# Kernel optimization log

Hardware: AMD Instinct MI355X
Metric: run time of the kernel (lower is better)

## Reference

```python
import jax, jax.numpy as jnp
import numpy as np

DIM = 64
HEADS = 8
GLOBAL_HEADS = 4   # heads - local_attn_heads
DIM_HEAD = 64
INNER = HEADS * DIM_HEAD  # 512
NB_FEATURES = int(DIM_HEAD * np.log(DIM_HEAD))  # 266, performer_pytorch default
NUM_TOKENS = 64
VOCAB = 26
B, N = 8, 2048


def _orth_gauss(m, d, rng):
    # gaussian orthogonal random matrix (scaling=0), as in performer_pytorch
    blocks = []
    for _ in range(int(np.ceil(m / d))):
        q, _ = np.linalg.qr(rng.normal(size=(d, d)))
        blocks.append(q.T)
    mat = np.concatenate(blocks, 0)[:m]
    mult = np.linalg.norm(rng.normal(size=(m, d)), axis=1)
    return (mult[:, None] * mat).astype(np.float32)


def _layernorm(x, g, b, eps=1e-5):
    mu = x.mean(-1, keepdims=True)
    var = jnp.mean((x - mu) ** 2, axis=-1, keepdims=True)
    return (x - mu) / jnp.sqrt(var + eps) * g + b


def _fixed_pos_emb(n, dim):
    inv_freq = 1.0 / (10000.0 ** (jnp.arange(0, dim, 2, dtype=jnp.float32) / dim))
    t = jnp.arange(n, dtype=jnp.float32)[:, None] * inv_freq[None, :]
    return jnp.concatenate([jnp.sin(t), jnp.cos(t)], axis=-1)  # [n, dim]


def _rotate_every_two(x):
    x1, x2 = x[..., ::2], x[..., 1::2]
    return jnp.stack((-x2, x1), axis=-1).reshape(x.shape)


def _apply_rotary(q, k, sinu):
    half = sinu.shape[-1] // 2
    sin = jnp.repeat(sinu[:, :half], 2, axis=-1)
    cos = jnp.repeat(sinu[:, half:], 2, axis=-1)
    rot = lambda t: t * cos + _rotate_every_two(t) * sin
    return rot(q), rot(k)


def _softmax_kernel(x, proj, is_query, eps=1e-4):
    # FAVOR+ positive softmax random features
    dn = x.shape[-1] ** -0.25
    ratio = proj.shape[0] ** -0.5
    dash = jnp.einsum('bhnd,md->bhnm', x * dn, proj)
    diag = jnp.sum(x * x, axis=-1, keepdims=True) * (0.5 * dn * dn)
    mx = jnp.max(dash, axis=-1, keepdims=True) if is_query else jnp.max(dash)
    return ratio * (jnp.exp(dash - diag - mx) + eps)


def _forward(input_ids, tok_emb, ln1_g, ln1_b, Wq, Wk, Wv, Wo, ln2_g, ln2_b,
             W1, b1, W2, b2, lnf_g, lnf_b, Wout, bout, Wc1, bc1, Wc2, bc2, proj):
    b, n = input_ids.shape
    mask = input_ids != 0  # padding mask (pad id == 0)
    x = tok_emb[input_ids] + _fixed_pos_emb(n, DIM)[None]  # token + abs sinusoidal pos
    sinu = _fixed_pos_emb(n, DIM_HEAD)  # rotary table for attention heads

    def attn(h):
        hn = _layernorm(h, ln1_g, ln1_b)
        to_h = lambda W: (hn @ W).reshape(b, n, HEADS, DIM_HEAD).transpose(0, 2, 1, 3)
        q, k, v = to_h(Wq), to_h(Wk), to_h(Wv)  # [b,h,n,d]
        qg, ql = q[:, :GLOBAL_HEADS], q[:, GLOBAL_HEADS:]
        kg, kl = k[:, :GLOBAL_HEADS], k[:, GLOBAL_HEADS:]
        vg, vl = v[:, :GLOBAL_HEADS], v[:, GLOBAL_HEADS:]
        # --- global heads: FAVOR+ linear attention (rotary applied to global q/k only) ---
        vg = vg * mask[:, None, :, None]  # performer zeroes v at padded positions
        qg, kg = _apply_rotary(qg, kg, sinu)
        qp = _softmax_kernel(qg, proj, True)   # [b,h,n,m]
        kp = _softmax_kernel(kg, proj, False)
        ctx = jnp.einsum('bhnm,bhnd->bhmd', kp, vg)
        denom = jnp.einsum('bhnm,bhm->bhn', qp, kp.sum(axis=2))
        og = jnp.einsum('bhnm,bhmd->bhnd', qp, ctx) / denom[..., None]
        # --- local heads: window_size == seq_len -> exact softmax attn + key pad mask ---
        dots = jnp.einsum('bhnd,bhmd->bhnm', ql, kl) * (DIM_HEAD ** -0.5)
        dots = jnp.where(mask[:, None, None, :], dots, jnp.asarray(-1e9, dots.dtype))
        ol = jnp.einsum('bhnm,bhmd->bhnd', jax.nn.softmax(dots, axis=-1), vl)
        out = jnp.concatenate([og, ol], axis=1).transpose(0, 2, 1, 3).reshape(b, n, INNER)
        return out @ Wo

    def ff(h):
        hn = _layernorm(h, ln2_g, ln2_b)
        return jax.nn.gelu(hn @ W1 + b1, approximate=False) @ W2 + b2

    # reversible sequence, depth 1: x1 = x2 = x; output = mean of the two streams
    y1 = x + attn(x)
    y2 = x + ff(y1)
    h = _layernorm(0.5 * (y1 + y2), lnf_g, lnf_b)
    logits = h @ Wout + bout  # [b, n, NUM_TOKENS]
    rep = logits[:, 0, :]     # CLS slot, [b, 64]
    out = jax.nn.relu(rep @ Wc1 + bc1) @ Wc2 + bc2  # [b, 2]
    return out, rep


def setup_inputs():
    key = jax.random.key(0)
    ks = jax.random.split(key, 12)
    rng = np.random.default_rng(0)
    s = lambda k, shape, scale=0.05: jax.random.normal(k, shape, jnp.float32) * scale
    return {
        'input_ids': jax.random.randint(ks[0], (B, N), 0, VOCAB, dtype=jnp.int32),
        'tok_emb': s(ks[1], (NUM_TOKENS, DIM), 1.0),
        'ln1_g': jnp.ones((DIM,), jnp.float32), 'ln1_b': jnp.zeros((DIM,), jnp.float32),
        'Wq': s(ks[2], (DIM, INNER)), 'Wk': s(ks[3], (DIM, INNER)), 'Wv': s(ks[4], (DIM, INNER)),
        'Wo': s(ks[5], (INNER, DIM)),
        'ln2_g': jnp.ones((DIM,), jnp.float32), 'ln2_b': jnp.zeros((DIM,), jnp.float32),
        'W1': s(ks[6], (DIM, 4 * DIM)), 'b1': jnp.zeros((4 * DIM,), jnp.float32),
        'W2': s(ks[7], (4 * DIM, DIM)), 'b2': jnp.zeros((DIM,), jnp.float32),
        'lnf_g': jnp.ones((DIM,), jnp.float32), 'lnf_b': jnp.zeros((DIM,), jnp.float32),
        'Wout': s(ks[8], (DIM, NUM_TOKENS)), 'bout': jnp.zeros((NUM_TOKENS,), jnp.float32),
        'Wc1': s(ks[9], (DIM, 32)), 'bc1': jnp.zeros((32,), jnp.float32),
        'Wc2': s(ks[10], (32, 2)), 'bc2': jnp.zeros((2,), jnp.float32),
        'proj': jnp.asarray(_orth_gauss(NB_FEATURES, DIM_HEAD, rng)),
    }


def reference(input_ids, tok_emb, ln1_g, ln1_b, Wq, Wk, Wv, Wo, ln2_g, ln2_b,
              W1, b1, W2, b2, lnf_g, lnf_b, Wout, bout, Wc1, bc1, Wc2, bc2, proj):
    return _forward(input_ids, tok_emb, ln1_g, ln1_b, Wq, Wk, Wv, Wo, ln2_g, ln2_b,
                    W1, b1, W2, b2, lnf_g, lnf_b, Wout, bout, Wc1, bc1, Wc2, bc2, proj)
```

## Files before the change

### kernel.cpp

```cpp
#include <hip/hip_runtime.h>
#include <math.h>

#define NTOK 2048
#define NBF 266
#define MPAD 272
#define ZWORDS4 138323u

typedef unsigned short u16;
typedef __attribute__((ext_vector_type(8))) short short8;
typedef __attribute__((ext_vector_type(4))) float f32x4;

__device__ __forceinline__ float bf2f(u16 u) {
  unsigned int x = ((unsigned int)u) << 16;
  return __uint_as_float(x);
}
__device__ __forceinline__ u16 f2bf(float f) {
  unsigned int x = __float_as_uint(f);
  unsigned int r = x + 0x7FFFu + ((x >> 16) & 1u);
  return (u16)(r >> 16);
}
__device__ __forceinline__ float wredsum64(float v) {
  for (int o = 32; o > 0; o >>= 1) v += __shfl_xor(v, o);
  return v;
}
__device__ __forceinline__ float bsum256(float v, float* red) {
  for (int o = 32; o > 0; o >>= 1) v += __shfl_xor(v, o);
  __syncthreads();
  if ((threadIdx.x & 63) == 0) red[threadIdx.x >> 6] = v;
  __syncthreads();
  return red[0] + red[1] + red[2] + red[3];
}
__device__ __forceinline__ float bmax256(float v, float* red) {
  for (int o = 32; o > 0; o >>= 1) v = fmaxf(v, __shfl_xor(v, o));
  __syncthreads();
  if ((threadIdx.x & 63) == 0) red[threadIdx.x >> 6] = v;
  __syncthreads();
  return fmaxf(fmaxf(red[0], red[1]), fmaxf(red[2], red[3]));
}
#define INVF_C 0.4152410118609190f

__global__ __launch_bounds__(128) void k_prep(
    const int* __restrict__ ids, const float* __restrict__ tok_emb,
    const float* __restrict__ ln1g, const float* __restrict__ ln1b,
    const float* __restrict__ Wk, const float* __restrict__ Wv,
    u16* __restrict__ Kg, u16* __restrict__ Vg, u16* __restrict__ hng,
    float* __restrict__ diagK, float* __restrict__ x0,
    uint4* __restrict__ zbase) {
  int blk = blockIdx.x;
  int b = blk >> 8, nt = blk & 255;
  int n0 = nt * 8;
  int t = threadIdx.x;
  int w = t >> 6, lane = t & 63;
  __shared__ float hn[8][64];
  __shared__ float idm[8];
  __shared__ float2 sctab[256];

  {
    unsigned int zi = (unsigned int)blk * 128u + (unsigned int)t;
    if (zi < ZWORDS4) zbase[zi] = make_uint4(0u, 0u, 0u, 0u);
  }
#pragma unroll
  for (int p = 0; p < 2; ++p) {
    int ee = t + p * 128;
    int n = n0 + (ee >> 5), i = ee & 31;
    float ang = (float)n * exp2f(-INVF_C * (float)i);
    sctab[ee] = make_float2(sinf(ang), cosf(ang));
  }
  __syncthreads();

  float g = ln1g[lane], bb = ln1b[lane];
#pragma unroll
  for (int j2 = 0; j2 < 4; ++j2) {
    int j = w * 4 + j2;
    int n = n0 + j;
    int id = ids[b * NTOK + n];
    float2 p = sctab[(j << 5) + (lane & 31)];
    float pv = (lane < 32) ? p.x : p.y;
    float xv = tok_emb[id * 64 + lane] + pv;
    float mu = wredsum64(xv) * 0.015625f;
    float dv = xv - mu;
    float var = wredsum64(dv * dv) * 0.015625f;
    float hv = dv * rsqrtf(var + 1e-5f) * g + bb;
    hn[j][lane] = hv;
    hng[((size_t)b * NTOK + n) * 64 + lane] = f2bf(hv);
    if (lane == 0) idm[j] = (id != 0) ? 1.f : 0.f;
    if (n == 0) x0[b * 64 + lane] = xv;
  }
  __syncthreads();

  float acc[8][4];
#pragma unroll
  for (int j = 0; j < 8; ++j)
#pragma unroll
    for (int i = 0; i < 4; ++i) acc[j][i] = 0.f;
  const float* wsrc = (t < 64) ? (Wk + t * 4) : (Wv + (t - 64) * 4);
  for (int d2 = 0; d2 < 64; ++d2) {
    float4 w0 = *reinterpret_cast<const float4*>(wsrc + d2 * 512);
#pragma unroll
    for (int j = 0; j < 8; ++j) {
      float hv = hn[j][d2];
      acc[j][0] += hv * w0.x; acc[j][1] += hv * w0.y;
      acc[j][2] += hv * w0.z; acc[j][3] += hv * w0.w;
    }
  }

  if (t < 64) {
    int hh = t >> 4, db = (t & 15) * 4;
    int i0 = (t & 15) * 2;
#pragma unroll
    for (int j = 0; j < 8; ++j) {
      int n = n0 + j;
      float2 t0 = sctab[(j << 5) + i0];
      float2 t1 = sctab[(j << 5) + i0 + 1];
      float s0 = t0.x, c0 = t0.y, s1 = t1.x, c1 = t1.y;
      float kr0 = acc[j][0] * c0 - acc[j][1] * s0;
      float kr1 = acc[j][1] * c0 + acc[j][0] * s0;
      float kr2 = acc[j][2] * c1 - acc[j][3] * s1;
      float kr3 = acc[j][3] * c1 + acc[j][2] * s1;
      float dq = kr0 * kr0 + kr1 * kr1 + kr2 * kr2 + kr3 * kr3;
      dq += __shfl_xor(dq, 1);
      dq += __shfl_xor(dq, 2);
      dq += __shfl_xor(dq, 4);
      dq += __shfl_xor(dq, 8);
      size_t hb = (size_t)(b * 4 + hh) * NTOK + n;
      if ((t & 15) == 0) diagK[hb] = dq * 0.0625f;
      ushort4 s;
      s.x = f2bf(kr0); s.y = f2bf(kr1); s.z = f2bf(kr2); s.w = f2bf(kr3);
      *reinterpret_cast<ushort4*>(Kg + hb * 64 + db) = s;
    }
  } else {
    int tv = t - 64;
    int hh = tv >> 4, db = (tv & 15) * 4;
#pragma unroll
    for (int j = 0; j < 8; ++j) {
      int n = n0 + j;
      float m = idm[j];
      ushort4 vv;
      vv.x = f2bf(acc[j][0] * m); vv.y = f2bf(acc[j][1] * m);
      vv.z = f2bf(acc[j][2] * m); vv.w = f2bf(acc[j][3] * m);
      *reinterpret_cast<ushort4*>(
          Vg + ((size_t)(b * 4 + hh) * NTOK + n) * 64 + db) = vv;
    }
  }
}

__device__ __forceinline__ void stage_prj(const float* __restrict__ proj,
                                          u16* prjbf, int t, int m0, int rows) {
  for (int c = t; c < rows * 8; c += 256) {
    int r = c >> 3, k0 = (c & 7) * 8;
    int m = m0 + r;
    int e = (r * 64 + k0) ^ ((r & 7) << 3);
    uint4 pk;
    if (m < NBF) {
      const float4* ps = reinterpret_cast<const float4*>(proj + m * 64 + k0);
      float4 p0 = ps[0], p1 = ps[1];
      pk.x = (unsigned)f2bf(p0.x) | ((unsigned)f2bf(p0.y) << 16);
      pk.y = (unsigned)f2bf(p0.z) | ((unsigned)f2bf(p0.w) << 16);
      pk.z = (unsigned)f2bf(p1.x) | ((unsigned)f2bf(p1.y) << 16);
      pk.w = (unsigned)f2bf(p1.z) | ((unsigned)f2bf(p1.w) << 16);
    } else {
      pk.x = pk.y = pk.z = pk.w = 0u;
    }
    *reinterpret_cast<uint4*>(&prjbf[e]) = pk;
  }
}

__global__ __launch_bounds__(256) void k_max(
    const u16* __restrict__ Kg, const float* __restrict__ proj,
    unsigned int* __restrict__ gmax) {
  int bh = blockIdx.x, ns = blockIdx.y;
  int t = threadIdx.x, lane = t & 63, w = t >> 6;
  __shared__ __align__(16) u16 prjbf[MPAD * 64];
  __shared__ __align__(16) u16 kbf[64 * 64];
  __shared__ float red[4];
  stage_prj(proj, prjbf, t, 0, MPAD);
  float mv = -3e38f;
  int ko = (lane >> 4) * 8;
  for (int c4 = 0; c4 < 2; ++c4) {
    int nb = ns * 128 + c4 * 64;
    __syncthreads();
    for (int p = 0; p < 2; ++p) {
      int idx = t + p * 256;
      int n = idx >> 3, k0 = (idx & 7) * 8;
      uint4 src = *reinterpret_cast<const uint4*>(
          Kg + ((size_t)bh * NTOK + nb + n) * 64 + k0);
      *reinterpret_cast<uint4*>(&kbf[(n * 64 + k0) ^ ((n & 7) << 3)]) = src;
    }
    __syncthreads();
    int nl = w * 16 + (lane & 15);
    short8 a0 = *reinterpret_cast<const short8*>(&kbf[(nl * 64 + ko) ^ ((nl & 7) << 3)]);
    short8 a1 = *reinterpret_cast<const short8*>(&kbf[(nl * 64 + ko + 32) ^ ((nl & 7) << 3)]);
#pragma unroll
    for (int mt = 0; mt < 17; ++mt) {
      int m = mt * 16 + (lane & 15);
      short8 b0 = *reinterpret_cast<const short8*>(&prjbf[(m * 64 + ko) ^ ((m & 7) << 3)]);
      short8 b1 = *reinterpret_cast<const short8*>(&prjbf[(m * 64 + ko + 32) ^ ((m & 7) << 3)]);
      f32x4 d = {0.f, 0.f, 0.f, 0.f};
      d = __builtin_amdgcn_mfma_f32_16x16x32_bf16(a0, b0, d, 0, 0, 0);
      d = __builtin_amdgcn_mfma_f32_16x16x32_bf16(a1, b1, d, 0, 0, 0);
      if (m < NBF) {
        mv = fmaxf(mv, fmaxf(fmaxf(d[0], d[1]), fmaxf(d[2], d[3])));
      }
    }
  }
  mv *= 0.35355339059327373f;
  for (int o = 32; o > 0; o >>= 1) mv = fmaxf(mv, __shfl_xor(mv, o));
  __syncthreads();
  if (lane == 0) red[w] = mv;
  __syncthreads();
  if (t == 0) {
    float m2 = fmaxf(fmaxf(red[0], red[1]), fmaxf(red[2], red[3]));
    unsigned int b = __float_as_uint(m2);
    unsigned int u = (b & 0x80000000u) ? ~b : (b | 0x80000000u);
    atomicMax(gmax, u);
  }
}

__global__ __launch_bounds__(256) void k_ctx(
    const u16* __restrict__ Kg, const u16* __restrict__ Vg,
    const float* __restrict__ diagK, const float* __restrict__ proj,
    const unsigned int* __restrict__ gmax,
    float* __restrict__ ctx, float* __restrict__ ksum) {
  int bh = blockIdx.x, ns = blockIdx.y, mz = blockIdx.z;
  int m0 = mz * 144;
  int nmt = mz ? 8 : 9;
  int t = threadIdx.x, lane = t & 63, w = t >> 6;
  __shared__ __align__(16) u16 prjbf[144 * 64];
  __shared__ __align__(16) u16 kpT[144 * 64];
  __shared__ __align__(16) u16 kbf[64 * 64];
  __shared__ __align__(16) u16 vbT[64 * 64];
  __shared__ float dg[64];
  __shared__ float ksl[144];
  stage_prj(proj, prjbf, t, m0, 144);
  if (t < 144) ksl[t] = 0.f;
  unsigned int u = *gmax;
  unsigned int bb = (u & 0x80000000u) ? (u & 0x7FFFFFFFu) : ~u;
  float mx = __uint_as_float(bb);
  const float dn = 0.35355339059327373f;
  const float ratio = 1.0f / sqrtf(266.0f);
  int ko = (lane >> 4) * 8;
  f32x4 acc[9];
  float ksacc[9];
#pragma unroll
  for (int i = 0; i < 9; ++i) { acc[i] = (f32x4){0.f, 0.f, 0.f, 0.f}; ksacc[i] = 0.f; }

  for (int c4 = 0; c4 < 4; ++c4) {
    int nb = ns * 256 + c4 * 64;
    for (int p = 0; p < 2; ++p) {
      int idx = t + p * 256;
      int n = idx >> 3, k0 = (idx & 7) * 8;
      uint4 src = *reinterpret_cast<const uint4*>(
          Kg + ((size_t)bh * NTOK + nb + n) * 64 + k0);
      *reinterpret_cast<uint4*>(&kbf[(n * 64 + k0) ^ ((n & 7) << 3)]) = src;
      uint4 vv = *reinterpret_cast<const uint4*>(
          Vg + ((size_t)bh * NTOK + nb + n) * 64 + k0);
      u16 pv[8];
      *reinterpret_cast<uint4*>(pv) = vv;
#pragma unroll
      for (int i = 0; i < 8; ++i) {
        int d = k0 + i;
        vbT[(d * 64 + n) ^ ((d & 7) << 3)] = pv[i];
      }
    }
    if (t < 64) dg[t] = diagK[(size_t)bh * NTOK + nb + t];
    __syncthreads();
    {
      int nl = w * 16 + (lane & 15);
      short8 a0 = *reinterpret_cast<const short8*>(&kbf[(nl * 64 + ko) ^ ((nl & 7) << 3)]);
      short8 a1 = *reinterpret_cast<const short8*>(&kbf[(nl * 64 + ko + 32) ^ ((nl & 7) << 3)]);
      float dgv[4];
#pragma unroll
      for (int r = 0; r < 4; ++r) dgv[r] = dg[w * 16 + (lane >> 4) * 4 + r];
      int n0 = w * 16 + (lane >> 4) * 4;
#pragma unroll
      for (int mt = 0; mt < 9; ++mt) {
        if (mt < nmt) {
          int lr = mt * 16 + (lane & 15);
          short8 b0 = *reinterpret_cast<const short8*>(&prjbf[(lr * 64 + ko) ^ ((lr & 7) << 3)]);
          short8 b1 = *reinterpret_cast<const short8*>(&prjbf[(lr * 64 + ko + 32) ^ ((lr & 7) << 3)]);
          f32x4 d = {0.f, 0.f, 0.f, 0.f};
          d = __builtin_amdgcn_mfma_f32_16x16x32_bf16(a0, b0, d, 0, 0, 0);
          d = __builtin_amdgcn_mfma_f32_16x16x32_bf16(a1, b1, d, 0, 0, 0);
          float kp0 = ratio * (expf(dn * d[0] - dgv[0] - mx) + 1e-4f);
          float kp1 = ratio * (expf(dn * d[1] - dgv[1] - mx) + 1e-4f);
          float kp2 = ratio * (expf(dn * d[2] - dgv[2] - mx) + 1e-4f);
          float kp3 = ratio * (expf(dn * d[3] - dgv[3] - mx) + 1e-4f);
          ushort4 pkk;
          pkk.x = f2bf(kp0); pkk.y = f2bf(kp1); pkk.z = f2bf(kp2); pkk.w = f2bf(kp3);
          *reinterpret_cast<ushort4*>(&kpT[(lr * 64 + n0) ^ ((lr & 7) << 3)]) = pkk;
          float ksp = kp0 + kp1 + kp2 + kp3;
          ksp += __shfl_xor(ksp, 16);
          ksp += __shfl_xor(ksp, 32);
          ksacc[mt] += ksp;
        }
      }
    }
    __syncthreads();
    {
      int dcol = w * 16 + (lane & 15);
      short8 vb0 = *reinterpret_cast<const short8*>(&vbT[(dcol * 64 + ko) ^ ((dcol & 7) << 3)]);
      short8 vb1 = *reinterpret_cast<const short8*>(&vbT[(dcol * 64 + ko + 32) ^ ((dcol & 7) << 3)]);
#pragma unroll
      for (int mt = 0; mt < 9; ++mt) {
        if (mt < nmt) {
          int lr = mt * 16 + (lane & 15);
          short8 a0 = *reinterpret_cast<const short8*>(&kpT[(lr * 64 + ko) ^ ((lr & 7) << 3)]);
          short8 a1 = *reinterpret_cast<const short8*>(&kpT[(lr * 64 + ko + 32) ^ ((lr & 7) << 3)]);
          acc[mt] = __builtin_amdgcn_mfma_f32_16x16x32_bf16(a0, vb0, acc[mt], 0, 0, 0);
          acc[mt] = __builtin_amdgcn_mfma_f32_16x16x32_bf16(a1, vb1, acc[mt], 0, 0, 0);
        }
      }
    }
    __syncthreads();
  }
  int dcol = w * 16 + (lane & 15);
#pragma unroll
  for (int mt = 0; mt < 9; ++mt) {
    if (mt < nmt) {
#pragma unroll
      for (int r = 0; r < 4; ++r) {
        int m = m0 + mt * 16 + (lane >> 4) * 4 + r;
        if (m < NBF)
          atomicAdd(&ctx[((size_t)bh * NBF + m) * 64 + dcol], acc[mt][r]);
      }
      if (lane < 16) atomicAdd(&ksl[mt * 16 + lane], ksacc[mt]);
    }
  }
  __syncthreads();
  if (t < 144 && m0 + t < NBF)
    atomicAdd(&ksum[(size_t)bh * NBF + m0 + t], ksl[t]);
}

__global__ __launch_bounds__(256) void k_att(
    const int* __restrict__ ids,
    const float* __restrict__ ln1g, const float* __restrict__ ln1b,
    const float* __restrict__ Wq, const float* __restrict__ Wk,
    const float* __restrict__ Wv, const float* __restrict__ proj,
    const u16* __restrict__ hng,
    const float* __restrict__ ctx, const float* __restrict__ ksum,
    const float* __restrict__ x0,
    const float* __restrict__ ln2g, const float* __restrict__ ln2b,
    const float* __restrict__ Wo,
    const float* __restrict__ W1, const float* __restrict__ b1,
    const float* __restrict__ W2, const float* __restrict__ b2,
    const float* __restrict__ lnfg, const float* __restrict__ lnfb,
    const float* __restrict__ Wout, const float* __restrict__ bout,
    const float* __restrict__ Wc1, const float* __restrict__ bc1,
    const float* __restrict__ Wc2, const float* __restrict__ bc2,
    float* __restrict__ att, unsigned int* __restrict__ cnt,
    float* __restrict__ out) {
  int b = blockIdx.x, h = blockIdx.y;
  int t = threadIdx.x;
  int lane = t & 63, wg = t >> 6;
  __shared__ float hn1[64], qh[64], qpart[4][64], red[4], pol[4][64];
  __shared__ float buf[272];
  __shared__ float dots[2048];
  __shared__ float wkq[64], svec[64];
  __shared__ u16 vst[512 * 64];
  __shared__ int lastf;
  __shared__ float fo512[512], fx0[64], fy1[64], fhn2[64], fgact[256];
  __shared__ float fhfin[64], frep[64], fc1[32];
  const float dn = 0.35355339059327373f;
  const float ratio = 1.0f / sqrtf(266.0f);

  if (t < 64) {
    float xv = x0[b * 64 + t];
    float mu = wredsum64(xv) * 0.015625f;
    float dv = xv - mu;
    float var = wredsum64(dv * dv) * 0.015625f;
    hn1[t] = dv * rsqrtf(var + 1e-5f) * ln1g[t] + ln1b[t];
  }
  __syncthreads();
  {
    float p = 0;
#pragma unroll
    for (int dd = 0; dd < 16; ++dd)
      p += hn1[wg * 16 + dd] * Wq[(wg * 16 + dd) * 512 + h * 64 + lane];
    qpart[wg][lane] = p;
  }
  __syncthreads();
  if (t < 64) qh[t] = qpart[0][t] + qpart[1][t] + qpart[2][t] + qpart[3][t];
  __syncthreads();

  if (h < 4) {
    int bh = b * 4 + h;
    float dq = 0;
#pragma unroll
    for (int d = 0; d < 64; ++d) dq += qh[d] * qh[d];
    dq *= 0.0625f;
    float lmax = -3e38f;
#pragma unroll
    for (int pass = 0; pass < 2; ++pass) {
      int m = t + pass * 256;
      if (m < NBF) {
        const float4* pp = reinterpret_cast<const float4*>(proj + m * 64);
        float s = 0;
#pragma unroll
        for (int q4 = 0; q4 < 16; ++q4) {
          float4 uu = pp[q4];
          s += qh[q4 * 4] * uu.x + qh[q4 * 4 + 1] * uu.y +
               qh[q4 * 4 + 2] * uu.z + qh[q4 * 4 + 3] * uu.w;
        }
        float dash = dn * s;
        buf[m] = dash;
        lmax = fmaxf(lmax, dash);
      }
    }
    float mxq = bmax256(lmax, red);
    float part = 0;
#pragma unroll
    for (int pass = 0; pass < 2; ++pass) {
      int m = t + pass * 256;
      if (m < NBF) {
        float qp = ratio * (expf(buf[m] - dq - mxq) + 1e-4f);
        buf[m] = qp;
        part += qp * ksum[(size_t)bh * NBF + m];
      }
    }
    float den = bsum256(part, red);
    __syncthreads();
    {
      float s = 0;
      for (int m = wg; m < NBF; m += 4)
        s += buf[m] * ctx[((size_t)bh * NBF + m) * 64 + lane];
      pol[wg][lane] = s;
    }
    __syncthreads();
    if (t < 64)
      att[b * 512 + h * 64 + t] =
          (pol[0][t] + pol[1][t] + pol[2][t] + pol[3][t]) / den;
  } else {
    int ch = h * 64;
    if (t < 64) {
      float s = 0;
#pragma unroll 8
      for (int j = 0; j < 64; ++j) s += Wk[t * 512 + ch + j] * qh[j];
      wkq[t] = s;
    }
    __syncthreads();
    const u16* hnb = hng + (size_t)b * NTOK * 64;
    float lmax = -3e38f;
#pragma unroll
    for (int i = 0; i < 8; ++i) {
      int n1 = t + i * 256;
      const ushort4* hr = reinterpret_cast<const ushort4*>(hnb + (size_t)n1 * 64);
      float s = 0;
#pragma unroll
      for (int d4 = 0; d4 < 16; ++d4) {
        ushort4 uu = hr[d4];
        s += wkq[d4 * 4] * bf2f(uu.x) + wkq[d4 * 4 + 1] * bf2f(uu.y) +
             wkq[d4 * 4 + 2] * bf2f(uu.z) + wkq[d4 * 4 + 3] * bf2f(uu.w);
      }
      float dv = s * 0.125f;
      if (ids[b * NTOK + n1] == 0) dv = -1e9f;
      dots[n1] = dv;
      lmax = fmaxf(lmax, dv);
    }
    float mxl = bmax256(lmax, red);
    float ps = 0;
#pragma unroll
    for (int i = 0; i < 8; ++i) {
      int n1 = t + i * 256;
      float p = expf(dots[n1] - mxl);
      dots[n1] = p;
      ps += p;
    }
    float sden = bsum256(ps, red);
    float acc = 0;
    for (int c = 0; c < 4; ++c) {
      __syncthreads();
      const ushort4* src = reinterpret_cast<const ushort4*>(hnb + (size_t)(c * 512) * 64);
      ushort4* dst = reinterpret_cast<ushort4*>(vst);
#pragma unroll
      for (int i = 0; i < 32; ++i) dst[t + i * 256] = src[t + i * 256];
      __syncthreads();
      int r0 = wg * 128;
#pragma unroll 8
      for (int r = 0; r < 128; ++r)
        acc += dots[c * 512 + r0 + r] * bf2f(vst[(r0 + r) * 64 + lane]);
    }
    __syncthreads();
    pol[wg][lane] = acc;
    __syncthreads();
    if (t < 64) svec[t] = pol[0][t] + pol[1][t] + pol[2][t] + pol[3][t];
    __syncthreads();
    {
      float p2 = 0;
#pragma unroll
      for (int dd = 0; dd < 16; ++dd)
        p2 += svec[wg * 16 + dd] * Wv[(wg * 16 + dd) * 512 + ch + lane];
      pol[wg][lane] = p2;
    }
    __syncthreads();
    if (t < 64)
      att[b * 512 + h * 64 + t] =
          (pol[0][t] + pol[1][t] + pol[2][t] + pol[3][t]) / sden;
  }

  __syncthreads();
  if (t == 0) {
    __threadfence();
    unsigned int prev = atomicAdd(&cnt[b], 1u);
    lastf = (prev == 7u) ? 1 : 0;
  }
  __syncthreads();
  if (!lastf) return;
  __threadfence();

  fo512[t] = att[b * 512 + t];
  fo512[t + 256] = att[b * 512 + t + 256];
  if (t < 64) fx0[t] = x0[b * 64 + t];
  __syncthreads();
  {
    float s = 0;
#pragma unroll 4
    for (int c = wg * 128; c < wg * 128 + 128; ++c) s += fo512[c] * Wo[c * 64 + lane];
    pol[wg][lane] = s;
  }
  __syncthreads();
  if (t < 64) {
    float yv = fx0[t] + pol[0][t] + pol[1][t] + pol[2][t] + pol[3][t];
    fy1[t] = yv;
    float mu = wredsum64(yv) * 0.015625f;
    float dv = yv - mu;
    float var = wredsum64(dv * dv) * 0.015625f;
    fhn2[t] = dv * rsqrtf(var + 1e-5f) * ln2g[t] + ln2b[t];
  }
  __syncthreads();
  {
    float s = b1[t];
#pragma unroll 4
    for (int d = 0; d < 64; ++d) s += fhn2[d] * W1[d * 256 + t];
    fgact[t] = 0.5f * s * (1.f + erff(s * 0.7071067811865475f));
  }
  __syncthreads();
  {
    float s = 0;
#pragma unroll 4
    for (int j = wg * 64; j < wg * 64 + 64; ++j) s += fgact[j] * W2[j * 64 + lane];
    pol[wg][lane] = s;
  }
  __syncthreads();
  if (t < 64) {
    float y2 = fx0[t] + b2[t] + pol[0][t] + pol[1][t] + pol[2][t] + pol[3][t];
    float hm = 0.5f * (fy1[t] + y2);
    float mu = wredsum64(hm) * 0.015625f;
    float dv = hm - mu;
    float var = wredsum64(dv * dv) * 0.015625f;
    fhfin[t] = dv * rsqrtf(var + 1e-5f) * lnfg[t] + lnfb[t];
  }
  __syncthreads();
  {
    float s = 0;
#pragma unroll
    for (int dd = 0; dd < 16; ++dd)
      s += fhfin[wg * 16 + dd] * Wout[(wg * 16 + dd) * 64 + lane];
    pol[wg][lane] = s;
  }
  __syncthreads();
  if (t < 64) {
    float s = bout[t] + pol[0][t] + pol[1][t] + pol[2][t] + pol[3][t];
    frep[t] = s;
    out[16 + b * 64 + t] = s;
  }
  __syncthreads();
  if (t < 32) {
    float s = bc1[t];
#pragma unroll 4
    for (int d = 0; d < 64; ++d) s += frep[d] * Wc1[d * 32 + t];
    fc1[t] = fmaxf(s, 0.f);
  }
  __syncthreads();
  if (t < 2) {
    float s = bc2[t];
#pragma unroll
    for (int jj = 0; jj < 32; ++jj) s += fc1[jj] * Wc2[jj * 2 + t];
    out[b * 2 + t] = s;
  }
}

extern "C" void kernel_launch(void* const* d_in, const int* in_sizes, int n_in,
                              void* d_out, int out_size, void* d_ws, size_t ws_size,
                              hipStream_t stream) {
  (void)in_sizes; (void)n_in; (void)out_size; (void)ws_size;
  const int* ids = (const int*)d_in[0];
  const float* tok = (const float*)d_in[1];
  const float* ln1g = (const float*)d_in[2];
  const float* ln1b = (const float*)d_in[3];
  const float* Wq = (const float*)d_in[4];
  const float* Wk = (const float*)d_in[5];
  const float* Wv = (const float*)d_in[6];
  const float* Wo = (const float*)d_in[7];
  const float* ln2g = (const float*)d_in[8];
  const float* ln2b = (const float*)d_in[9];
  const float* W1 = (const float*)d_in[10];
  const float* b1 = (const float*)d_in[11];
  const float* W2 = (const float*)d_in[12];
  const float* b2 = (const float*)d_in[13];
  const float* lnfg = (const float*)d_in[14];
  const float* lnfb = (const float*)d_in[15];
  const float* Wout = (const float*)d_in[16];
  const float* bout = (const float*)d_in[17];
  const float* Wc1 = (const float*)d_in[18];
  const float* bc1 = (const float*)d_in[19];
  const float* Wc2 = (const float*)d_in[20];
  const float* bc2 = (const float*)d_in[21];
  const float* proj = (const float*)d_in[22];

  uint8_t* w = (uint8_t*)d_ws;
  size_t off = 0;
  const size_t big = (size_t)8 * 4 * NTOK * 64 * 2;
  u16* Kg = (u16*)(w + off); off += big;
  u16* Vg = (u16*)(w + off); off += big;
  u16* hng = (u16*)(w + off); off += (size_t)8 * NTOK * 64 * 2;
  float* diagK = (float*)(w + off); off += (size_t)8 * 4 * NTOK * 4;
  float* ctx = (float*)(w + off); off += (size_t)8 * 4 * NBF * 64 * 4;
  float* ksum = (float*)(w + off); off += (size_t)8 * 4 * NBF * 4;
  unsigned int* gmax = (unsigned int*)(w + off); off += 4;
  unsigned int* cnt = (unsigned int*)(w + off); off += 32;
  off += 12;
  float* x0 = (float*)(w + off); off += 64 * 8 * 4;
  float* att = (float*)(w + off); off += (size_t)8 * 512 * 4;

  k_prep<<<8 * 256, 128, 0, stream>>>(ids, tok, ln1g, ln1b, Wk, Wv, Kg, Vg, hng,
                                      diagK, x0, (uint4*)ctx);
  k_max<<<dim3(32, 16), 256, 0, stream>>>(Kg, proj, gmax);
  k_ctx<<<dim3(32, 8, 2), 256, 0, stream>>>(Kg, Vg, diagK, proj, gmax, ctx, ksum);
  k_att<<<dim3(8, 8), 256, 0, stream>>>(ids, ln1g, ln1b, Wq, Wk, Wv, proj, hng,
                                        ctx, ksum, x0, ln2g, ln2b, Wo, W1, b1,
                                        W2, b2, lnfg, lnfb, Wout, bout, Wc1,
                                        bc1, Wc2, bc2, att, cnt, (float*)d_out);
}
```

Baseline: 115.2 us.

## Split local-attention heads across four sequence chunks with atomic partial reductions

```diff
diff --git a/kernel.cpp b/kernel.cpp
--- a/kernel.cpp
+++ b/kernel.cpp
@@ -4,7 +4,7 @@
 #define NTOK 2048
 #define NBF 266
 #define MPAD 272
-#define ZWORDS4 138323u
+#define ZWORDS4 138843u
 
 typedef unsigned short u16;
 typedef __attribute__((ext_vector_type(8))) short short8;
@@ -347,21 +347,22 @@
     const float* __restrict__ Wout, const float* __restrict__ bout,
     const float* __restrict__ Wc1, const float* __restrict__ bc1,
     const float* __restrict__ Wc2, const float* __restrict__ bc2,
-    float* __restrict__ att, unsigned int* __restrict__ cnt,
+    float* __restrict__ att, float* __restrict__ svecG,
+    float* __restrict__ sdenG, unsigned int* __restrict__ cnt,
     float* __restrict__ out) {
-  int b = blockIdx.x, h = blockIdx.y;
-  int t = threadIdx.x;
-  int lane = t & 63, wg = t >> 6;
+  int b = blockIdx.x, y = blockIdx.y;
+  int t = threadIdx.x, lane = t & 63, wg = t >> 6;
   __shared__ float hn1[64], qh[64], qpart[4][64], red[4], pol[4][64];
   __shared__ float buf[272];
-  __shared__ float dots[2048];
-  __shared__ float wkq[64], svec[64];
-  __shared__ u16 vst[512 * 64];
+  __shared__ __align__(16) u16 vst[512 * 64];
+  __shared__ float pbuf[512];
+  __shared__ float wkq[64];
   __shared__ int lastf;
   __shared__ float fo512[512], fx0[64], fy1[64], fhn2[64], fgact[256];
-  __shared__ float fhfin[64], frep[64], fc1[32];
+  __shared__ float fhfin[64], frep[64], fc1[32], fsd[4];
   const float dn = 0.35355339059327373f;
   const float ratio = 1.0f / sqrtf(266.0f);
+  int h = (y < 4) ? y : (4 + ((y - 4) >> 2));
 
   if (t < 64) {
     float xv = x0[b * 64 + t];
@@ -382,7 +383,7 @@
   if (t < 64) qh[t] = qpart[0][t] + qpart[1][t] + qpart[2][t] + qpart[3][t];
   __syncthreads();
 
-  if (h < 4) {
+  if (y < 4) {
     int bh = b * 4 + h;
     float dq = 0;
 #pragma unroll
@@ -430,86 +431,83 @@
       att[b * 512 + h * 64 + t] =
           (pol[0][t] + pol[1][t] + pol[2][t] + pol[3][t]) / den;
   } else {
-    int ch = h * 64;
-    if (t < 64) {
+    int hl = (y - 4) >> 2, sl = (y - 4) & 3;
+    int ch = (4 + hl) * 64;
+    {
+      float p = 0;
+#pragma unroll
+      for (int jj = 0; jj < 16; ++jj)
+        p += Wk[lane * 512 + ch + wg * 16 + jj] * qh[wg * 16 + jj];
+      qpart[wg][lane] = p;
+    }
+    __syncthreads();
+    if (t < 64) wkq[t] = qpart[0][t] + qpart[1][t] + qpart[2][t] + qpart[3][t];
+    const u16* hnb = hng + ((size_t)b * NTOK + sl * 512) * 64;
+    for (int p = 0; p < 16; ++p) {
+      int idx = t + p * 256;
+      int r = idx >> 3, k0 = (idx & 7) * 8;
+      uint4 src = *reinterpret_cast<const uint4*>(hnb + (size_t)r * 64 + k0);
+      *reinterpret_cast<uint4*>(&vst[(r * 64 + k0) ^ ((r & 7) << 3)]) = src;
+    }
+    __syncthreads();
+    float ps = 0;
+#pragma unroll
+    for (int i = 0; i < 2; ++i) {
+      int r = t + i * 256;
       float s = 0;
+#pragma unroll
+      for (int c8 = 0; c8 < 8; ++c8) {
+        uint4 uu = *reinterpret_cast<const uint4*>(
+            &vst[(r * 64 + c8 * 8) ^ ((r & 7) << 3)]);
+        u16 pv[8];
+        *reinterpret_cast<uint4*>(pv) = uu;
+#pragma unroll
+        for (int k = 0; k < 8; ++k) s += wkq[c8 * 8 + k] * bf2f(pv[k]);
+      }
+      float p = (ids[b * NTOK + sl * 512 + r] == 0) ? 0.f : expf(s * 0.125f);
+      pbuf[r] = p;
+      ps += p;
+    }
+    float psb = bsum256(ps, red);
+    if (t == 0) atomicAdd(&sdenG[b * 4 + hl], psb);
+    float acc = 0;
+    int r0 = wg * 128;
 #pragma unroll 8
-      for (int j = 0; j < 64; ++j) s += Wk[t * 512 + ch + j] * qh[j];
-      wkq[t] = s;
-    }
-    __syncthreads();
-    const u16* hnb = hng + (size_t)b * NTOK * 64;
-    float lmax = -3e38f;
-#pragma unroll
-    for (int i = 0; i < 8; ++i) {
-      int n1 = t + i * 256;
-      const ushort4* hr = reinterpret_cast<const ushort4*>(hnb + (size_t)n1 * 64);
-      float s = 0;
-#pragma unroll
-      for (int d4 = 0; d4 < 16; ++d4) {
-        ushort4 uu = hr[d4];
-        s += wkq[d4 * 4] * bf2f(uu.x) + wkq[d4 * 4 + 1] * bf2f(uu.y) +
-             wkq[d4 * 4 + 2] * bf2f(uu.z) + wkq[d4 * 4 + 3] * bf2f(uu.w);
-      }
-      float dv = s * 0.125f;
-      if (ids[b * NTOK + n1] == 0) dv = -1e9f;
-      dots[n1] = dv;
-      lmax = fmaxf(lmax, dv);
-    }
-    float mxl = bmax256(lmax, red);
-    float ps = 0;
-#pragma unroll
-    for (int i = 0; i < 8; ++i) {
-      int n1 = t + i * 256;
-      float p = expf(dots[n1] - mxl);
-      dots[n1] = p;
-      ps += p;
-    }
-    float sden = bsum256(ps, red);
-    float acc = 0;
-    for (int c = 0; c < 4; ++c) {
-      __syncthreads();
-      const ushort4* src = reinterpret_cast<const ushort4*>(hnb + (size_t)(c * 512) * 64);
-      ushort4* dst = reinterpret_cast<ushort4*>(vst);
-#pragma unroll
-      for (int i = 0; i < 32; ++i) dst[t + i * 256] = src[t + i * 256];
-      __syncthreads();
-      int r0 = wg * 128;
-#pragma unroll 8
-      for (int r = 0; r < 128; ++r)
-        acc += dots[c * 512 + r0 + r] * bf2f(vst[(r0 + r) * 64 + lane]);
-    }
-    __syncthreads();
+    for (int r = 0; r < 128; ++r)
+      acc += pbuf[r0 + r] * bf2f(vst[((r0 + r) * 64 + lane) ^ (((r0 + r) & 7) << 3)]);
     pol[wg][lane] = acc;
     __syncthreads();
-    if (t < 64) svec[t] = pol[0][t] + pol[1][t] + pol[2][t] + pol[3][t];
-    __syncthreads();
-    {
-      float p2 = 0;
-#pragma unroll
-      for (int dd = 0; dd < 16; ++dd)
-        p2 += svec[wg * 16 + dd] * Wv[(wg * 16 + dd) * 512 + ch + lane];
-      pol[wg][lane] = p2;
-    }
-    __syncthreads();
     if (t < 64)
-      att[b * 512 + h * 64 + t] =
-          (pol[0][t] + pol[1][t] + pol[2][t] + pol[3][t]) / sden;
+      atomicAdd(&svecG[(b * 4 + hl) * 64 + t],
+                pol[0][t] + pol[1][t] + pol[2][t] + pol[3][t]);
   }
 
   __syncthreads();
   if (t == 0) {
     __threadfence();
     unsigned int prev = atomicAdd(&cnt[b], 1u);
-    lastf = (prev == 7u) ? 1 : 0;
+    lastf = (prev == 19u) ? 1 : 0;
   }
   __syncthreads();
   if (!lastf) return;
   __threadfence();
 
-  fo512[t] = att[b * 512 + t];
-  fo512[t + 256] = att[b * 512 + t + 256];
+  if (t < 4) fsd[t] = sdenG[b * 4 + t];
+  {
+    int hh = t >> 6, j = t & 63;
+    float s = 0;
+#pragma unroll 8
+    for (int d = 0; d < 64; ++d)
+      s += svecG[(b * 4 + hh) * 64 + d] * Wv[d * 512 + 256 + hh * 64 + j];
+    pol[hh][j] = s;
+  }
+  if (t < 256) fo512[t] = att[b * 512 + t];
   if (t < 64) fx0[t] = x0[b * 64 + t];
+  __syncthreads();
+  {
+    int hh = t >> 6, j = t & 63;
+    fo512[256 + hh * 64 + j] = pol[hh][j] / fsd[hh];
+  }
   __syncthreads();
   {
     float s = 0;
@@ -616,6 +614,8 @@
   float* diagK = (float*)(w + off); off += (size_t)8 * 4 * NTOK * 4;
   float* ctx = (float*)(w + off); off += (size_t)8 * 4 * NBF * 64 * 4;
   float* ksum = (float*)(w + off); off += (size_t)8 * 4 * NBF * 4;
+  float* svecG = (float*)(w + off); off += (size_t)8 * 4 * 64 * 4;
+  float* sdenG = (float*)(w + off); off += (size_t)8 * 4 * 4;
   unsigned int* gmax = (unsigned int*)(w + off); off += 4;
   unsigned int* cnt = (unsigned int*)(w + off); off += 32;
   off += 12;
@@ -626,8 +626,9 @@
                                       diagK, x0, (uint4*)ctx);
   k_max<<<dim3(32, 16), 256, 0, stream>>>(Kg, proj, gmax);
   k_ctx<<<dim3(32, 8, 2), 256, 0, stream>>>(Kg, Vg, diagK, proj, gmax, ctx, ksum);
-  k_att<<<dim3(8, 8), 256, 0, stream>>>(ids, ln1g, ln1b, Wq, Wk, Wv, proj, hng,
-                                        ctx, ksum, x0, ln2g, ln2b, Wo, W1, b1,
-                                        W2, b2, lnfg, lnfb, Wout, bout, Wc1,
-                                        bc1, Wc2, bc2, att, cnt, (float*)d_out);
-}
+  k_att<<<dim3(8, 20), 256, 0, stream>>>(ids, ln1g, ln1b, Wq, Wk, Wv, proj, hng,
+                                         ctx, ksum, x0, ln2g, ln2b, Wo, W1, b1,
+                                         W2, b2, lnfg, lnfb, Wout, bout, Wc1,
+                                         bc1, Wc2, bc2, att, svecG, sdenG, cnt,
+                                         (float*)d_out);
+}
```

Result: no change. 114.8 us (-0.3%).
